# Kernel tuning notes

Measured on AMD Instinct MI355X. Metric: run time of the kernel, lower is better.

Reference implementation:

```python
import jax, jax.numpy as jnp
import numpy as np

# ---- problem sizes ----
N_NEURONS = 1536
N_INPUTS = 768
BATCH = 32
T = 256
DT = 1.0  # ms per step
SURRGRAD_SCALE = 10.0

# ---- per-cell-type physiology (recurrent): 0=excitatory, 1=inhibitory ----
CELL_TAU_MEM = np.array([20.0, 10.0], np.float32)   # ms
CELL_THETA   = np.array([-50.0, -50.0], np.float32) # mV
CELL_URESET  = np.array([-65.0, -65.0], np.float32) # mV
CELL_EL      = np.array([-65.0, -65.0], np.float32) # mV
CELL_GL      = np.array([10.0, 10.0], np.float32)   # nS
CELL_TAUREF  = np.array([2.0, 1.0], np.float32)     # ms

# ---- synapse types: AMPA(pre=exc), NMDA(pre=exc), GABA_A(pre=inh) ----
SYN_CELL_ID   = np.array([0, 0, 1], np.int32)
SYN_TAU_RISE  = np.array([0.5, 2.0, 0.5], np.float32)
SYN_TAU_DECAY = np.array([2.0, 100.0, 5.0], np.float32)
SYN_EREV      = np.array([0.0, 0.0, -70.0], np.float32)
SYN_GBAR      = np.array([1.0, 0.5, 1.0], np.float32)

# ---- feedforward: single excitatory input type, single AMPA synapse ----
FF_TAU_RISE, FF_TAU_DECAY, FF_EREV, FF_GBAR = 0.5, 2.0, 0.0, 1.0


@jax.custom_vjp
def spike(v):
    # Heaviside spike with fast-sigmoid surrogate gradient
    return (v >= 0).astype(v.dtype)

def _spike_fwd(v):
    return spike(v), v

def _spike_bwd(v, g):
    return (g / (SURRGRAD_SCALE * jnp.abs(v) + 1.0) ** 2,)

spike.defvjp(_spike_fwd, _spike_bwd)


def setup_inputs() -> dict:
    key = jax.random.key(0)
    ks = jax.random.split(key, 6)
    input_spikes = (jax.random.uniform(ks[0], (BATCH, T, N_INPUTS)) < 0.05).astype(jnp.float32)
    weights = jax.random.normal(ks[1], (N_NEURONS, N_NEURONS), jnp.float32) * 0.05
    weights_FF = jax.random.normal(ks[2], (N_INPUTS, N_NEURONS), jnp.float32) * 0.05
    cell_type_indices = jax.random.randint(ks[3], (N_NEURONS,), 0, 2, jnp.int32)
    cell_type_indices_FF = jnp.zeros((N_INPUTS,), jnp.int32)
    scaling_factors = jax.random.uniform(ks[4], (2, 2), jnp.float32, 0.5, 1.5)
    scaling_factors_FF = jax.random.uniform(ks[5], (1, 2), jnp.float32, 0.5, 1.5)
    return {
        'input_spikes': input_spikes,
        'weights': weights,
        'weights_FF': weights_FF,
        'scaling_factors': scaling_factors,
        'scaling_factors_FF': scaling_factors_FF,
        'cell_type_indices': cell_type_indices,
        'cell_type_indices_FF': cell_type_indices_FF,
    }


def _simulate(input_spikes, weights, weights_FF, scaling_factors, scaling_factors_FF,
              cell_type_indices, cell_type_indices_FF):
    ct = cell_type_indices
    B = input_spikes.shape[0]

    # per-neuron physiology gathered by cell type
    tau_mem = jnp.asarray(CELL_TAU_MEM)[ct]
    theta = jnp.asarray(CELL_THETA)[ct]
    u_reset = jnp.asarray(CELL_URESET)[ct]
    e_l = jnp.asarray(CELL_EL)[ct]
    g_l = jnp.asarray(CELL_GL)[ct]
    ref_steps = jnp.asarray(CELL_TAUREF)[ct] / DT
    leak_coef = DT / (tau_mem * g_l)  # dt / C_m

    # effective weights: cell-type scaling + presynaptic synapse-type mask
    sf = scaling_factors[ct[:, None], ct[None, :]]            # (N, N)
    W = weights * sf
    pre_mask = (jnp.asarray(SYN_CELL_ID)[:, None] == ct[None, :]).astype(W.dtype)  # (S, N)
    Ws = W[None, :, :] * pre_mask[:, :, None]                  # (S, N, N)
    sfF = scaling_factors_FF[cell_type_indices_FF[:, None], ct[None, :]]
    WF = weights_FF * sfF                                      # (n_in, N)

    alpha_r = jnp.exp(-DT / jnp.asarray(SYN_TAU_RISE))[:, None, None]   # (S,1,1)
    alpha_d = jnp.exp(-DT / jnp.asarray(SYN_TAU_DECAY))[:, None, None]
    arF = jnp.exp(jnp.float32(-DT / FF_TAU_RISE))
    adF = jnp.exp(jnp.float32(-DT / FF_TAU_DECAY))
    gbar = jnp.asarray(SYN_GBAR)
    gbarE = jnp.asarray(SYN_GBAR * SYN_EREV)
    S = gbar.shape[0]

    U0 = jnp.broadcast_to(e_l, (B, N_NEURONS))
    carry0 = (U0,
              jnp.zeros((B, N_NEURONS), jnp.float32),       # previous spikes
              jnp.zeros((S, B, N_NEURONS), jnp.float32),    # x (rise)
              jnp.zeros((S, B, N_NEURONS), jnp.float32),    # g (decay)
              jnp.zeros((B, N_NEURONS), jnp.float32),       # x_FF
              jnp.zeros((B, N_NEURONS), jnp.float32),       # g_FF
              jnp.zeros((B, N_NEURONS), jnp.float32))       # refractory counter

    def step(carry, I_t):
        U, s_prev, x, g, xF, gF, ref = carry
        # dual-exponential conductance update per synapse type
        inp = jnp.einsum('bn,snm->sbm', s_prev, Ws)
        x = alpha_r * x + inp
        g = alpha_d * g + x
        xF = arF * xF + I_t @ WF
        gF = adF * gF + xF
        # conductance-based synaptic current: sum_s gbar_s * g_s * (E_s - U)
        gtot = jnp.einsum('s,sbn->bn', gbar, g) + FF_GBAR * gF
        gE = jnp.einsum('s,sbn->bn', gbarE, g) + (FF_GBAR * FF_EREV) * gF
        I_syn = gE - gtot * U
        # leaky membrane integration
        U_new = U + leak_coef * (g_l * (e_l - U) + I_syn)
        # refractory clamp
        in_ref = ref > 0
        U_new = jnp.where(in_ref, u_reset, U_new)
        ref = jnp.maximum(ref - 1.0, 0.0)
        # surrogate-gradient spike and reset
        s_new = spike(U_new - theta)
        U_out = jnp.where(s_new > 0, u_reset, U_new)
        ref = jnp.where(s_new > 0, ref_steps, ref)
        return (U_out, s_new, x, g, xF, gF, ref), (s_new, U_out)

    I_seq = jnp.transpose(input_spikes, (1, 0, 2))  # (T, B, n_in)
    _, (spk, volts) = jax.lax.scan(step, carry0, I_seq)
    return jnp.transpose(spk, (1, 0, 2)), jnp.transpose(volts, (1, 0, 2))


def reference(input_spikes, weights, weights_FF, scaling_factors, scaling_factors_FF,
              cell_type_indices, cell_type_indices_FF):
    return _simulate(input_spikes, weights, weights_FF, scaling_factors, scaling_factors_FF,
                     cell_type_indices, cell_type_indices_FF)
```

## Files before the change

kernel.cpp:

```cpp
#include <hip/hip_runtime.h>
#include <stdint.h>


__global__ __launch_bounds__(768) void snn_lif_kernel(
    const float* __restrict__ I,
    const float* __restrict__ W,
    const float* __restrict__ WF,
    const float* __restrict__ sf,
    const float* __restrict__ sfF,
    const int*   __restrict__ ct,
    float* __restrict__ out,
    uint64_t* __restrict__ recpub)
{
    const int tid = threadIdx.x;
    const int j   = blockIdx.x & 7;
    const int b   = blockIdx.x >> 3;
    const int wv  = tid >> 6;
    const int wl  = tid & 63;

    __shared__ float4   part0[2][12][48];
    __shared__ float4   part1[2][12][48];
    __shared__ float4   partF[2][12][48];
    __shared__ uint32_t ctm32_sh[48];

    for (int r = 0; r < 2; ++r) {
        int c = ct[r * 768 + tid];
        uint64_t bal = __ballot(c != 0);
        if (wl == 0) {
            ctm32_sh[r * 24 + wv * 2]     = (uint32_t)bal;
            ctm32_sh[r * 24 + wv * 2 + 1] = (uint32_t)(bal >> 32);
        }
    }
    __syncthreads();

    const int m = j * 192 + ((tid < 192) ? tid : 0);
    const int   myct = ct[m];
    const float s0m  = sf[myct];
    const float s1m  = sf[2 + myct];
    const float sFm  = sfF[myct];
    const float lc   = (myct == 0) ? (1.0f / 200.0f) : (1.0f / 100.0f);
    const float refsteps = (myct == 0) ? 2.0f : 1.0f;
    const float ar0 = expf(-1.0f / 0.5f),  ad0 = expf(-1.0f / 2.0f);
    const float ar1 = expf(-1.0f / 2.0f),  ad1 = expf(-1.0f / 100.0f);
    const float ar2 = expf(-1.0f / 0.5f),  ad2 = expf(-1.0f / 5.0f);
    const float arF = expf(-1.0f / 0.5f),  adF = expf(-1.0f / 2.0f);

    float U = -65.0f, refc = 0.0f;
    float x0 = 0, g0 = 0, x1 = 0, g1 = 0, x2 = 0, g2 = 0, xF = 0, gF = 0;

    const int  btbase  = b * 256;
    const bool gl      = (wl < 48);
    const uint32_t colbase = (uint32_t)(j * 192 + wl * 4);

    uint64_t fmask;
    {
        float iv = __builtin_nontemporal_load(
            &I[(uint32_t)btbase * 768u + (uint32_t)tid]);
        fmask = __ballot(iv > 0.5f);
    }

    for (int t = 0; t < 256; ++t) {
        float ivn = 0.0f;
        if (t < 255)
            ivn = __builtin_nontemporal_load(
                &I[(uint32_t)(btbase + t + 1) * 768u + (uint32_t)tid]);

        float4 a0 = make_float4(0.f, 0.f, 0.f, 0.f);
        float4 a1 = a0, aF = a0;

        {
            uint64_t mm = fmask;
            while (mm) {
                const int bit = __builtin_ctzll(mm);
                mm &= mm - 1;
                const uint32_t row = (uint32_t)(wv * 64 + bit);
                if (gl) {
                    const float4 w = *(const float4*)(WF + row * 1536u + colbase);
                    aF.x += w.x; aF.y += w.y; aF.z += w.z; aF.w += w.w;
                }
            }
        }

        if (t > 0) {
            uint32_t ready = 0;
            const uint32_t pbase = (uint32_t)(btbase + t - 1) * 48u + (uint32_t)(wv * 4);
            do {
                uint64_t pv = 0;
                if (wl < 4)
                    pv = __hip_atomic_load(&recpub[pbase + (uint32_t)wl],
                                           __ATOMIC_RELAXED, __HIP_MEMORY_SCOPE_AGENT);
                const uint32_t plo = (uint32_t)pv;
                const uint32_t phi = (uint32_t)(pv >> 32);
                #pragma unroll
                for (int k = 0; k < 4; ++k) {
                    if (ready & (1u << k)) continue;
                    const uint32_t tg = __builtin_amdgcn_readlane(phi, k);
                    if (tg != (uint32_t)t) continue;
                    ready |= 1u << k;
                    uint32_t bits = __builtin_amdgcn_readlane(plo, k);
                    const uint32_t word = (uint32_t)(wv * 4 + k);
                    const uint32_t cm = ctm32_sh[word];
                    while (bits) {
                        const int bit = __builtin_ctz(bits);
                        bits &= bits - 1;
                        const uint32_t row = word * 32u + (uint32_t)bit;
                        if (gl) {
                            const float4 w = *(const float4*)(W + row * 1536u + colbase);
                            if ((cm >> bit) & 1u) {
                                a1.x += w.x; a1.y += w.y; a1.z += w.z; a1.w += w.w;
                            } else {
                                a0.x += w.x; a0.y += w.y; a0.z += w.z; a0.w += w.w;
                            }
                        }
                    }
                }
            } while (ready != 0xFu);
        }

        const int buf = t & 1;
        if (gl) {
            part0[buf][wv][wl] = a0;
            part1[buf][wv][wl] = a1;
            partF[buf][wv][wl] = aF;
        }
        fmask = __ballot(ivn > 0.5f);
        __syncthreads();

        if (tid < 192) {
            const float* p0 = (const float*)&part0[buf][0][0];
            const float* p1 = (const float*)&part1[buf][0][0];
            const float* pF = (const float*)&partF[buf][0][0];
            float z0s = 0.f, z1s = 0.f, zFs = 0.f;
            #pragma unroll
            for (int k = 0; k < 12; ++k) {
                z0s += p0[k * 192 + tid];
                z1s += p1[k * 192 + tid];
                zFs += pF[k * 192 + tid];
            }
            z0s *= s0m; z1s *= s1m; zFs *= sFm;
            x0 = ar0 * x0 + z0s;  g0 = ad0 * g0 + x0;
            x1 = ar1 * x1 + z0s;  g1 = ad1 * g1 + x1;
            x2 = ar2 * x2 + z1s;  g2 = ad2 * g2 + x2;
            xF = arF * xF + zFs;  gF = adF * gF + xF;
            const float gtot = g0 + 0.5f * g1 + g2 + gF;
            const float gE   = -70.0f * g2;
            const float Isyn = gE - gtot * U;
            float Un = U + lc * (10.0f * (-65.0f - U) + Isyn);
            if (refc > 0.0f) Un = -65.0f;
            refc = fmaxf(refc - 1.0f, 0.0f);
            const bool s = (Un - (-50.0f)) >= 0.0f;
            const uint64_t bal = __ballot(s);
            if (wl == 0 || wl == 32) {
                const uint32_t half = (wl == 0) ? (uint32_t)bal : (uint32_t)(bal >> 32);
                const uint32_t word = (uint32_t)(j * 6 + wv * 2) + (wl == 32 ? 1u : 0u);
                const uint32_t widx = (uint32_t)(btbase + t) * 48u + word;
                const uint64_t v = ((uint64_t)(uint32_t)(t + 1) << 32) | half;
                __hip_atomic_store(&recpub[widx], v, __ATOMIC_RELAXED,
                                   __HIP_MEMORY_SCOPE_AGENT);
            }
            const float Uo = s ? -65.0f : Un;
            refc = s ? refsteps : refc;
            U = Uo;
            const uint32_t oidx = (uint32_t)(btbase + t) * 1536u + (uint32_t)m;
            __builtin_nontemporal_store(s ? 1.0f : 0.0f, &out[oidx]);
            __builtin_nontemporal_store(Uo, &out[12582912u + oidx]);
        }
    }
}

extern "C" void kernel_launch(void* const* d_in, const int* in_sizes, int n_in,
                              void* d_out, int out_size, void* d_ws, size_t ws_size,
                              hipStream_t stream) {
    const float* I   = (const float*)d_in[0];
    const float* W   = (const float*)d_in[1];
    const float* WF  = (const float*)d_in[2];
    const float* sf  = (const float*)d_in[3];
    const float* sfF = (const float*)d_in[4];
    const int*   ct  = (const int*)d_in[5];

    uint64_t* recpub = (uint64_t*)d_ws;

    snn_lif_kernel<<<dim3(256), dim3(768), 0, stream>>>(
        I, W, WF, sf, sfF, ct, (float*)d_out, recpub);
}
```

Before: 750.9 us.

## Split work into single-wave blocks owning 64 neurons each, dropping LDS reduction

Each 768-thread block that owned 192 neurons and split the presynaptic rows across 12 waves is replaced by 768 single-wave blocks. Each wave owns 64 neurons and walks every active input and recurrent row itself, doing scalar gathers per column. This removes the shared-memory partial sums and the __syncthreads barrier each step, and the spike-word wait polls all 48 words with a single ballot. In exchange each wave issues many more serialized scalar loads per step, gives up float4 vectorization, and there are three times as many blocks spinning on the global flags.

```diff
diff --git a/kernel.cpp b/kernel.cpp
--- a/kernel.cpp
+++ b/kernel.cpp
@@ -2,7 +2,7 @@
 #include <stdint.h>
 
 
-__global__ __launch_bounds__(768) void snn_lif_kernel(
+__global__ __launch_bounds__(64) void snn_lif_kernel(
     const float* __restrict__ I,
     const float* __restrict__ W,
     const float* __restrict__ WF,
@@ -12,28 +12,22 @@
     float* __restrict__ out,
     uint64_t* __restrict__ recpub)
 {
-    const int tid = threadIdx.x;
-    const int j   = blockIdx.x & 7;
-    const int b   = blockIdx.x >> 3;
-    const int wv  = tid >> 6;
-    const int wl  = tid & 63;
+    const int wl  = threadIdx.x;
+    const int x   = blockIdx.x & 7;
+    const int k   = blockIdx.x >> 3;
+    const int b   = k / 3;
+    const int sub = k - 3 * b;
+    const int s   = 3 * x + sub;
+    const int m   = s * 64 + wl;
+    const int btbase = b * 256;
 
-    __shared__ float4   part0[2][12][48];
-    __shared__ float4   part1[2][12][48];
-    __shared__ float4   partF[2][12][48];
-    __shared__ uint32_t ctm32_sh[48];
+    uint32_t cmv = 0;
+    if (wl < 48) {
+        #pragma unroll
+        for (int i = 0; i < 32; ++i)
+            cmv |= (uint32_t)(ct[wl * 32 + i] != 0) << i;
+    }
 
-    for (int r = 0; r < 2; ++r) {
-        int c = ct[r * 768 + tid];
-        uint64_t bal = __ballot(c != 0);
-        if (wl == 0) {
-            ctm32_sh[r * 24 + wv * 2]     = (uint32_t)bal;
-            ctm32_sh[r * 24 + wv * 2 + 1] = (uint32_t)(bal >> 32);
-        }
-    }
-    __syncthreads();
-
-    const int m = j * 192 + ((tid < 192) ? tid : 0);
     const int   myct = ct[m];
     const float s0m  = sf[myct];
     const float s1m  = sf[2 + myct];
@@ -48,123 +42,104 @@
     float U = -65.0f, refc = 0.0f;
     float x0 = 0, g0 = 0, x1 = 0, g1 = 0, x2 = 0, g2 = 0, xF = 0, gF = 0;
 
-    const int  btbase  = b * 256;
-    const bool gl      = (wl < 48);
-    const uint32_t colbase = (uint32_t)(j * 192 + wl * 4);
-
-    uint64_t fmask;
+    float ivv[12];
     {
-        float iv = __builtin_nontemporal_load(
-            &I[(uint32_t)btbase * 768u + (uint32_t)tid]);
-        fmask = __ballot(iv > 0.5f);
+        const float* Ib = I + (uint32_t)btbase * 768u;
+        #pragma unroll
+        for (int c = 0; c < 12; ++c)
+            ivv[c] = __builtin_nontemporal_load(&Ib[c * 64 + wl]);
     }
 
+    const uint64_t need = 0x0000FFFFFFFFFFFFull;
+
     for (int t = 0; t < 256; ++t) {
-        float ivn = 0.0f;
-        if (t < 255)
-            ivn = __builtin_nontemporal_load(
-                &I[(uint32_t)(btbase + t + 1) * 768u + (uint32_t)tid]);
+        uint64_t fm[12];
+        #pragma unroll
+        for (int c = 0; c < 12; ++c) fm[c] = __ballot(ivv[c] > 0.5f);
 
-        float4 a0 = make_float4(0.f, 0.f, 0.f, 0.f);
-        float4 a1 = a0, aF = a0;
+        const uint64_t* pp = recpub + (uint32_t)(btbase + t - 1) * 48u;
+        uint64_t pv = 0;
+        if (t > 0 && wl < 48)
+            pv = __hip_atomic_load(pp + wl, __ATOMIC_RELAXED,
+                                   __HIP_MEMORY_SCOPE_AGENT);
 
-        {
-            uint64_t mm = fmask;
+        if (t < 255) {
+            const float* Ib = I + (uint32_t)(btbase + t + 1) * 768u;
+            #pragma unroll
+            for (int c = 0; c < 12; ++c)
+                ivv[c] = __builtin_nontemporal_load(&Ib[c * 64 + wl]);
+        }
+
+        float z0 = 0.f, z1 = 0.f, zF = 0.f;
+
+        #pragma unroll
+        for (int c = 0; c < 12; ++c) {
+            uint64_t mm = fm[c];
             while (mm) {
                 const int bit = __builtin_ctzll(mm);
                 mm &= mm - 1;
-                const uint32_t row = (uint32_t)(wv * 64 + bit);
-                if (gl) {
-                    const float4 w = *(const float4*)(WF + row * 1536u + colbase);
-                    aF.x += w.x; aF.y += w.y; aF.z += w.z; aF.w += w.w;
-                }
+                zF += WF[(uint32_t)(c * 64 + bit) * 1536u + (uint32_t)m];
             }
         }
 
         if (t > 0) {
-            uint32_t ready = 0;
-            const uint32_t pbase = (uint32_t)(btbase + t - 1) * 48u + (uint32_t)(wv * 4);
-            do {
-                uint64_t pv = 0;
-                if (wl < 4)
-                    pv = __hip_atomic_load(&recpub[pbase + (uint32_t)wl],
-                                           __ATOMIC_RELAXED, __HIP_MEMORY_SCOPE_AGENT);
-                const uint32_t plo = (uint32_t)pv;
-                const uint32_t phi = (uint32_t)(pv >> 32);
-                #pragma unroll
-                for (int k = 0; k < 4; ++k) {
-                    if (ready & (1u << k)) continue;
-                    const uint32_t tg = __builtin_amdgcn_readlane(phi, k);
-                    if (tg != (uint32_t)t) continue;
-                    ready |= 1u << k;
-                    uint32_t bits = __builtin_amdgcn_readlane(plo, k);
-                    const uint32_t word = (uint32_t)(wv * 4 + k);
-                    const uint32_t cm = ctm32_sh[word];
+            uint64_t done = 0;
+            for (;;) {
+                const uint64_t arr = __ballot((uint32_t)(pv >> 32) == (uint32_t)t);
+                uint64_t neww = arr & ~done;
+                done |= neww;
+                const uint32_t pvlo = (uint32_t)pv;
+                while (neww) {
+                    const int w = __builtin_ctzll(neww);
+                    neww &= neww - 1;
+                    uint32_t bits = __builtin_amdgcn_readlane(pvlo, w);
+                    const uint32_t cm = __builtin_amdgcn_readlane(cmv, w);
+                    const uint32_t rowbase = (uint32_t)w * 32u;
                     while (bits) {
                         const int bit = __builtin_ctz(bits);
                         bits &= bits - 1;
-                        const uint32_t row = word * 32u + (uint32_t)bit;
-                        if (gl) {
-                            const float4 w = *(const float4*)(W + row * 1536u + colbase);
-                            if ((cm >> bit) & 1u) {
-                                a1.x += w.x; a1.y += w.y; a1.z += w.z; a1.w += w.w;
-                            } else {
-                                a0.x += w.x; a0.y += w.y; a0.z += w.z; a0.w += w.w;
-                            }
-                        }
+                        const float wv_ = W[(rowbase + (uint32_t)bit) * 1536u + (uint32_t)m];
+                        if ((cm >> bit) & 1u) z1 += wv_;
+                        else                  z0 += wv_;
                     }
                 }
-            } while (ready != 0xFu);
+                if (done == need) break;
+                pv = 0;
+                if (wl < 48)
+                    pv = __hip_atomic_load(pp + wl, __ATOMIC_RELAXED,
+                                           __HIP_MEMORY_SCOPE_AGENT);
+            }
         }
 
-        const int buf = t & 1;
-        if (gl) {
-            part0[buf][wv][wl] = a0;
-            part1[buf][wv][wl] = a1;
-            partF[buf][wv][wl] = aF;
+        z0 *= s0m; z1 *= s1m; zF *= sFm;
+        x0 = ar0 * x0 + z0;  g0 = ad0 * g0 + x0;
+        x1 = ar1 * x1 + z0;  g1 = ad1 * g1 + x1;
+        x2 = ar2 * x2 + z1;  g2 = ad2 * g2 + x2;
+        xF = arF * xF + zF;  gF = adF * gF + xF;
+        const float gtot = g0 + 0.5f * g1 + g2 + gF;
+        const float gE   = -70.0f * g2;
+        const float Isyn = gE - gtot * U;
+        float Un = U + lc * (10.0f * (-65.0f - U) + Isyn);
+        if (refc > 0.0f) Un = -65.0f;
+        refc = fmaxf(refc - 1.0f, 0.0f);
+        const bool sp = (Un - (-50.0f)) >= 0.0f;
+
+        const uint64_t bal = __ballot(sp);
+        if (wl == 0 || wl == 32) {
+            const uint32_t bits = (wl == 0) ? (uint32_t)bal : (uint32_t)(bal >> 32);
+            const uint32_t widx = (uint32_t)(btbase + t) * 48u
+                                + (uint32_t)(s * 2) + (wl == 32 ? 1u : 0u);
+            const uint64_t v = ((uint64_t)(uint32_t)(t + 1) << 32) | bits;
+            __hip_atomic_store(&recpub[widx], v, __ATOMIC_RELAXED,
+                               __HIP_MEMORY_SCOPE_AGENT);
         }
-        fmask = __ballot(ivn > 0.5f);
-        __syncthreads();
 
-        if (tid < 192) {
-            const float* p0 = (const float*)&part0[buf][0][0];
-            const float* p1 = (const float*)&part1[buf][0][0];
-            const float* pF = (const float*)&partF[buf][0][0];
-            float z0s = 0.f, z1s = 0.f, zFs = 0.f;
-            #pragma unroll
-            for (int k = 0; k < 12; ++k) {
-                z0s += p0[k * 192 + tid];
-                z1s += p1[k * 192 + tid];
-                zFs += pF[k * 192 + tid];
-            }
-            z0s *= s0m; z1s *= s1m; zFs *= sFm;
-            x0 = ar0 * x0 + z0s;  g0 = ad0 * g0 + x0;
-            x1 = ar1 * x1 + z0s;  g1 = ad1 * g1 + x1;
-            x2 = ar2 * x2 + z1s;  g2 = ad2 * g2 + x2;
-            xF = arF * xF + zFs;  gF = adF * gF + xF;
-            const float gtot = g0 + 0.5f * g1 + g2 + gF;
-            const float gE   = -70.0f * g2;
-            const float Isyn = gE - gtot * U;
-            float Un = U + lc * (10.0f * (-65.0f - U) + Isyn);
-            if (refc > 0.0f) Un = -65.0f;
-            refc = fmaxf(refc - 1.0f, 0.0f);
-            const bool s = (Un - (-50.0f)) >= 0.0f;
-            const uint64_t bal = __ballot(s);
-            if (wl == 0 || wl == 32) {
-                const uint32_t half = (wl == 0) ? (uint32_t)bal : (uint32_t)(bal >> 32);
-                const uint32_t word = (uint32_t)(j * 6 + wv * 2) + (wl == 32 ? 1u : 0u);
-                const uint32_t widx = (uint32_t)(btbase + t) * 48u + word;
-                const uint64_t v = ((uint64_t)(uint32_t)(t + 1) << 32) | half;
-                __hip_atomic_store(&recpub[widx], v, __ATOMIC_RELAXED,
-                                   __HIP_MEMORY_SCOPE_AGENT);
-            }
-            const float Uo = s ? -65.0f : Un;
-            refc = s ? refsteps : refc;
-            U = Uo;
-            const uint32_t oidx = (uint32_t)(btbase + t) * 1536u + (uint32_t)m;
-            __builtin_nontemporal_store(s ? 1.0f : 0.0f, &out[oidx]);
-            __builtin_nontemporal_store(Uo, &out[12582912u + oidx]);
-        }
+        const float Uo = sp ? -65.0f : Un;
+        refc = sp ? refsteps : refc;
+        U = Uo;
+        const uint32_t oidx = (uint32_t)(btbase + t) * 1536u + (uint32_t)m;
+        __builtin_nontemporal_store(sp ? 1.0f : 0.0f, &out[oidx]);
+        __builtin_nontemporal_store(Uo, &out[12582912u + oidx]);
     }
 }
 
@@ -180,6 +155,6 @@
 
     uint64_t* recpub = (uint64_t*)d_ws;
 
-    snn_lif_kernel<<<dim3(256), dim3(768), 0, stream>>>(
+    snn_lif_kernel<<<dim3(768), dim3(64), 0, stream>>>(
         I, W, WF, sf, sfF, ct, (float*)d_out, recpub);
 }
```

Measured after the change: 2.061 ms. 2.74x slower.
